# Kernel tuning notes

Hardware: AMD Instinct MI355X
Metric: run time of the kernel (lower is better)

## Reference

```python
import jax, jax.numpy as jnp
import numpy as np

EPS = 1e-7  # keras.backend.epsilon()


def setup_inputs() -> dict:
    key = jax.random.key(0)
    k1, k2 = jax.random.split(key)
    B, S, D = 8, 1024, 768
    # scale down: module exponentiates raw dot products with no max-subtraction
    input_a = jax.random.normal(k1, (B, S, D), dtype=jnp.float32) * 0.05
    input_mask = jax.random.randint(k2, (B, S), 0, 2, dtype=jnp.int32)
    return {"input_a": input_a, "input_mask": input_mask}


def reference(input_a, input_mask):
    # e = exp(Q K^T) with Q = K = input_a, attend_type='dot' (no scaling)
    e = jnp.exp(jnp.einsum('bsd,btd->bst', input_a, input_a))  # [B,S,S]
    m = input_mask.astype(input_a.dtype)
    e = e * m[:, :, None] * m[:, None, :]  # mask rows and cols
    e = e / (jnp.sum(e, axis=-1, keepdims=True) + EPS)  # renormalize
    attend = jnp.einsum('bst,btd->bsd', e, input_a)  # V = input_a
    return attend
```

## Files before the change

### kernel.cpp

```cpp
#include <hip/hip_runtime.h>
#include <cstdint>
#include <cstddef>

#define BATCH 8
#define SEQ 1024
#define DIM 768
#define EPS_K 1e-7f

typedef __bf16 bf16x8 __attribute__((ext_vector_type(8)));
typedef float f32x4 __attribute__((ext_vector_type(4)));

__device__ __forceinline__ uint16_t f2bf(float f) {
  union { float f; uint32_t u; } v; v.f = f;
  uint32_t u = v.u;
  u += 0x7FFFu + ((u >> 16) & 1u);
  return (uint16_t)(u >> 16);
}

__device__ __forceinline__ void gload16(const void* g, void* l) {
  __builtin_amdgcn_global_load_lds(
      (const __attribute__((address_space(1))) uint32_t*)g,
      (__attribute__((address_space(3))) uint32_t*)l, 16, 0, 0);
}

__global__ __launch_bounds__(256) void convert_kernel(const float* __restrict__ A,
                                                      uint16_t* __restrict__ ab,
                                                      uint16_t* __restrict__ at) {
  const int b  = blockIdx.z;
  const int s0 = blockIdx.y * 64;
  const int d0 = blockIdx.x * 64;
  __shared__ uint16_t tl[64][66];
  const int c  = threadIdx.x & 63;
  const int r0 = threadIdx.x >> 6;
  const float* Ab = A + (size_t)b * SEQ * DIM;
  uint16_t* abb = ab + (size_t)b * SEQ * DIM;
#pragma unroll
  for (int i = 0; i < 16; ++i) {
    int r = r0 + i * 4;
    uint16_t h = f2bf(Ab[(size_t)(s0 + r) * DIM + d0 + c]);
    abb[(size_t)(s0 + r) * DIM + d0 + c] = h;
    tl[r][c] = h;
  }
  __syncthreads();
  uint16_t* atb = at + (size_t)b * DIM * SEQ;
#pragma unroll
  for (int i = 0; i < 16; ++i) {
    int r = r0 + i * 4;
    atb[(size_t)(d0 + r) * SEQ + s0 + c] = tl[c][r];
  }
}

__global__ __launch_bounds__(256) void scores_kernel(const uint16_t* __restrict__ ab,
                                                     const int* __restrict__ mask,
                                                     uint16_t* __restrict__ P) {
  const int b    = blockIdx.x & 7;
  const int tile = blockIdx.x >> 3;
  const int s0   = (tile >> 3) * 128;
  const int t0   = (tile & 7) * 128;

  const int tid  = threadIdx.x;
  const int lane = tid & 63;
  const int wid  = tid >> 6;
  const int wr   = wid >> 1;
  const int wc   = wid & 1;

  __shared__ uint16_t ldsQ[2][128 * 32];
  __shared__ uint16_t ldsK[2][128 * 32];
  __shared__ float mrow[128];
  __shared__ float mcol[128];

  if (tid < 128)        mrow[tid]       = (float)mask[b * SEQ + s0 + tid];
  else                  mcol[tid - 128] = (float)mask[b * SEQ + t0 + (tid - 128)];

  const uint16_t* aQ = ab + (size_t)b * SEQ * DIM + (size_t)s0 * DIM;
  const uint16_t* aK = ab + (size_t)b * SEQ * DIM + (size_t)t0 * DIM;

  const int sr = (tid * 8) >> 5;
  const int sc = (tid * 8) & 31;
#define STAGE(buf, k0)                                                         \
  do {                                                                         \
    int _i0 = tid * 8, _i1 = (256 + tid) * 8;                                  \
    gload16(aQ + (size_t)sr * DIM + (k0) + sc,        &ldsQ[buf][_i0]);        \
    gload16(aQ + (size_t)(sr + 64) * DIM + (k0) + sc, &ldsQ[buf][_i1]);        \
    gload16(aK + (size_t)sr * DIM + (k0) + sc,        &ldsK[buf][_i0]);        \
    gload16(aK + (size_t)(sr + 64) * DIM + (k0) + sc, &ldsK[buf][_i1]);        \
  } while (0)

  f32x4 acc[4][4];
#pragma unroll
  for (int m = 0; m < 4; ++m)
#pragma unroll
    for (int n = 0; n < 4; ++n) acc[m][n] = f32x4{0.f, 0.f, 0.f, 0.f};

  STAGE(0, 0);
  __syncthreads();

  const int rowQ = wr * 64 + (lane & 15);
  const int rowK = wc * 64 + (lane & 15);
  const int kch  = (lane >> 4) * 8;

  int cur = 0;
  for (int k0 = 0; k0 < DIM; k0 += 32) {
    if (k0 + 32 < DIM) STAGE(cur ^ 1, k0 + 32);

    bf16x8 qf[4], kf[4];
#pragma unroll
    for (int m = 0; m < 4; ++m) qf[m] = *(const bf16x8*)&ldsQ[cur][(rowQ + m * 16) * 32 + kch];
#pragma unroll
    for (int n = 0; n < 4; ++n) kf[n] = *(const bf16x8*)&ldsK[cur][(rowK + n * 16) * 32 + kch];
#pragma unroll
    for (int m = 0; m < 4; ++m)
#pragma unroll
      for (int n = 0; n < 4; ++n)
        acc[m][n] = __builtin_amdgcn_mfma_f32_16x16x32_bf16(qf[m], kf[n], acc[m][n], 0, 0, 0);

    __syncthreads();
    cur ^= 1;
  }
#undef STAGE

  uint16_t* Pb = P + (size_t)b * SEQ * SEQ;
#pragma unroll
  for (int m = 0; m < 4; ++m) {
    const int qb = wr * 64 + m * 16 + (lane >> 4) * 4;
#pragma unroll
    for (int n = 0; n < 4; ++n) {
      const int tloc = wc * 64 + n * 16 + (lane & 15);
      const float mc = mcol[tloc];
#pragma unroll
      for (int j = 0; j < 4; ++j) {
        float e = __expf(acc[m][n][j]) * mrow[qb + j] * mc;
        Pb[(size_t)(s0 + qb + j) * SEQ + t0 + tloc] = f2bf(e);
      }
    }
  }
}

__global__ __launch_bounds__(256) void out_kernel(const uint16_t* __restrict__ P,
                                                  const uint16_t* __restrict__ at,
                                                  float* __restrict__ out) {
  const int b    = blockIdx.x & 7;
  const int tile = blockIdx.x >> 3;
  const int q0   = (tile / 6) * 128;
  const int d0   = (tile % 6) * 128;

  const int tid  = threadIdx.x;
  const int lane = tid & 63;
  const int wid  = tid >> 6;
  const int wr   = wid >> 1;
  const int wc   = wid & 1;

  __shared__ uint16_t ldsP[2][128 * 32];
  __shared__ uint16_t ldsA[2][128 * 32];

  const uint16_t* Pb = P  + (size_t)b * SEQ * SEQ + (size_t)q0 * SEQ;
  const uint16_t* Ab = at + (size_t)b * DIM * SEQ + (size_t)d0 * SEQ;

  const int sr = (tid * 8) >> 5;
  const int sc = (tid * 8) & 31;
#define STAGE(buf, k0)                                                         \
  do {                                                                         \
    int _i0 = tid * 8, _i1 = (256 + tid) * 8;                                  \
    gload16(Pb + (size_t)sr * SEQ + (k0) + sc,        &ldsP[buf][_i0]);        \
    gload16(Pb + (size_t)(sr + 64) * SEQ + (k0) + sc, &ldsP[buf][_i1]);        \
    gload16(Ab + (size_t)sr * SEQ + (k0) + sc,        &ldsA[buf][_i0]);        \
    gload16(Ab + (size_t)(sr + 64) * SEQ + (k0) + sc, &ldsA[buf][_i1]);        \
  } while (0)

  f32x4 acc[4][4];
  f32x4 accd[4];
#pragma unroll
  for (int m = 0; m < 4; ++m) {
    accd[m] = f32x4{0.f, 0.f, 0.f, 0.f};
#pragma unroll
    for (int n = 0; n < 4; ++n) acc[m][n] = f32x4{0.f, 0.f, 0.f, 0.f};
  }

  bf16x8 onesf;
#pragma unroll
  for (int i = 0; i < 8; ++i) onesf[i] = (__bf16)1.0f;

  STAGE(0, 0);
  __syncthreads();

  const int rowP = wr * 64 + (lane & 15);
  const int rowA = wc * 64 + (lane & 15);
  const int kch  = (lane >> 4) * 8;

  int cur = 0;
  for (int k0 = 0; k0 < SEQ; k0 += 32) {
    if (k0 + 32 < SEQ) STAGE(cur ^ 1, k0 + 32);

    bf16x8 pf[4], af[4];
#pragma unroll
    for (int m = 0; m < 4; ++m) pf[m] = *(const bf16x8*)&ldsP[cur][(rowP + m * 16) * 32 + kch];
#pragma unroll
    for (int n = 0; n < 4; ++n) af[n] = *(const bf16x8*)&ldsA[cur][(rowA + n * 16) * 32 + kch];
#pragma unroll
    for (int m = 0; m < 4; ++m) {
#pragma unroll
      for (int n = 0; n < 4; ++n)
        acc[m][n] = __builtin_amdgcn_mfma_f32_16x16x32_bf16(pf[m], af[n], acc[m][n], 0, 0, 0);
      accd[m] = __builtin_amdgcn_mfma_f32_16x16x32_bf16(pf[m], onesf, accd[m], 0, 0, 0);
    }

    __syncthreads();
    cur ^= 1;
  }
#undef STAGE

  float* ob = out + (size_t)b * SEQ * DIM;
#pragma unroll
  for (int m = 0; m < 4; ++m) {
#pragma unroll
    for (int j = 0; j < 4; ++j) {
      const int ql = wr * 64 + m * 16 + (lane >> 4) * 4 + j;
      const float sc2 = 1.0f / (accd[m][j] + EPS_K);
#pragma unroll
      for (int n = 0; n < 4; ++n) {
        const int dl = d0 + wc * 64 + n * 16 + (lane & 15);
        ob[(size_t)(q0 + ql) * DIM + dl] = acc[m][n][j] * sc2;
      }
    }
  }
}

extern "C" void kernel_launch(void* const* d_in, const int* in_sizes, int n_in,
                              void* d_out, int out_size, void* d_ws, size_t ws_size,
                              hipStream_t stream) {
  (void)in_sizes; (void)n_in; (void)out_size; (void)ws_size;
  const float* A    = (const float*)d_in[0];
  const int*   mask = (const int*)d_in[1];
  float*       out  = (float*)d_out;

  char* ws = (char*)d_ws;
  const size_t NB_AB = (size_t)BATCH * SEQ * DIM * 2;
  const size_t NB_AT = NB_AB;
  uint16_t* ab = (uint16_t*)(ws);
  uint16_t* at = (uint16_t*)(ws + NB_AB);
  uint16_t* P  = (uint16_t*)(ws + NB_AB + NB_AT);

  dim3 blk(256);
  convert_kernel<<<dim3(DIM / 64, SEQ / 64, BATCH), blk, 0, stream>>>(A, ab, at);
  scores_kernel<<<dim3(64 * BATCH), blk, 0, stream>>>(ab, mask, P);
  out_kernel<<<dim3(48 * BATCH), blk, 0, stream>>>(P, at, out);
}
```

Baseline: 118.6 us.

## Enlarge GEMM tiles, swizzle LDS, deepen K step, vectorize conversion

Both GEMM kernels move to 512-thread blocks with 256x128 output tiles and a 64-wide K step. LDS columns are XOR-swizzled to avoid bank conflicts, and explicit vmcnt waits, raw barriers and setprio are meant to overlap the prefetch with MFMA work. The convert kernel now uses vectorized float4 loads and 16-byte bf16 stores for both the copy and the transpose. The grid shrinks to 256 and 192 blocks, which may underfill the 256 CUs, and the larger tiles raise register and LDS pressure.

```diff
diff --git a/kernel.cpp b/kernel.cpp
--- a/kernel.cpp
+++ b/kernel.cpp
@@ -9,6 +9,7 @@
 
 typedef __bf16 bf16x8 __attribute__((ext_vector_type(8)));
 typedef float f32x4 __attribute__((ext_vector_type(4)));
+typedef uint16_t u16x8 __attribute__((ext_vector_type(8)));
 
 __device__ __forceinline__ uint16_t f2bf(float f) {
   union { float f; uint32_t u; } v; v.f = f;
@@ -29,33 +30,41 @@
   const int b  = blockIdx.z;
   const int s0 = blockIdx.y * 64;
   const int d0 = blockIdx.x * 64;
-  __shared__ uint16_t tl[64][66];
-  const int c  = threadIdx.x & 63;
-  const int r0 = threadIdx.x >> 6;
-  const float* Ab = A + (size_t)b * SEQ * DIM;
-  uint16_t* abb = ab + (size_t)b * SEQ * DIM;
-#pragma unroll
-  for (int i = 0; i < 16; ++i) {
-    int r = r0 + i * 4;
-    uint16_t h = f2bf(Ab[(size_t)(s0 + r) * DIM + d0 + c]);
-    abb[(size_t)(s0 + r) * DIM + d0 + c] = h;
-    tl[r][c] = h;
+  __shared__ uint16_t tl[64][80];
+  const int tid = threadIdx.x;
+
+#pragma unroll
+  for (int i = 0; i < 2; ++i) {
+    const int sl = (tid >> 3) + i * 32;
+    const int ch = tid & 7;
+    const float* src = A + ((size_t)b * SEQ + s0 + sl) * DIM + d0 + ch * 8;
+    float4 f0 = *(const float4*)src;
+    float4 f1 = *(const float4*)(src + 4);
+    u16x8 h;
+    h[0] = f2bf(f0.x); h[1] = f2bf(f0.y); h[2] = f2bf(f0.z); h[3] = f2bf(f0.w);
+    h[4] = f2bf(f1.x); h[5] = f2bf(f1.y); h[6] = f2bf(f1.z); h[7] = f2bf(f1.w);
+    *(u16x8*)&ab[((size_t)b * SEQ + s0 + sl) * DIM + d0 + ch * 8] = h;
+    *(u16x8*)&tl[sl][ch * 8] = h;
   }
   __syncthreads();
-  uint16_t* atb = at + (size_t)b * DIM * SEQ;
-#pragma unroll
-  for (int i = 0; i < 16; ++i) {
-    int r = r0 + i * 4;
-    atb[(size_t)(d0 + r) * SEQ + s0 + c] = tl[c][r];
-  }
-}
-
-__global__ __launch_bounds__(256) void scores_kernel(const uint16_t* __restrict__ ab,
-                                                     const int* __restrict__ mask,
-                                                     uint16_t* __restrict__ P) {
+  const int dl = tid >> 2;
+#pragma unroll
+  for (int i = 0; i < 2; ++i) {
+    const int sc = (tid & 3) + i * 4;
+    u16x8 h;
+#pragma unroll
+    for (int e = 0; e < 8; ++e) h[e] = tl[sc * 8 + e][dl];
+    *(u16x8*)&at[((size_t)b * DIM + d0 + dl) * SEQ + s0 + sc * 8] = h;
+  }
+}
+
+
+__global__ __launch_bounds__(512, 2) void scores_kernel(const uint16_t* __restrict__ ab,
+                                                        const int* __restrict__ mask,
+                                                        uint16_t* __restrict__ P) {
   const int b    = blockIdx.x & 7;
   const int tile = blockIdx.x >> 3;
-  const int s0   = (tile >> 3) * 128;
+  const int s0   = (tile >> 3) * 256;
   const int t0   = (tile & 7) * 128;
 
   const int tid  = threadIdx.x;
@@ -64,26 +73,26 @@
   const int wr   = wid >> 1;
   const int wc   = wid & 1;
 
-  __shared__ uint16_t ldsQ[2][128 * 32];
-  __shared__ uint16_t ldsK[2][128 * 32];
-  __shared__ float mrow[128];
-  __shared__ float mcol[128];
-
-  if (tid < 128)        mrow[tid]       = (float)mask[b * SEQ + s0 + tid];
-  else                  mcol[tid - 128] = (float)mask[b * SEQ + t0 + (tid - 128)];
-
-  const uint16_t* aQ = ab + (size_t)b * SEQ * DIM + (size_t)s0 * DIM;
-  const uint16_t* aK = ab + (size_t)b * SEQ * DIM + (size_t)t0 * DIM;
-
-  const int sr = (tid * 8) >> 5;
-  const int sc = (tid * 8) & 31;
+  __shared__ __align__(16) uint16_t lA[2][256 * 64];
+  __shared__ __align__(16) uint16_t lB[2][128 * 64];
+
+  const uint16_t* gA = ab + ((size_t)b * SEQ + s0) * DIM;
+  const uint16_t* gB = ab + ((size_t)b * SEQ + t0) * DIM;
+
+  const int srl  = tid >> 3;
+  const int schx = ((tid & 7) ^ (srl & 7)) << 3;
+  const int sdst = srl * 64 + (tid & 7) * 8;
+
 #define STAGE(buf, k0)                                                         \
   do {                                                                         \
-    int _i0 = tid * 8, _i1 = (256 + tid) * 8;                                  \
-    gload16(aQ + (size_t)sr * DIM + (k0) + sc,        &ldsQ[buf][_i0]);        \
-    gload16(aQ + (size_t)(sr + 64) * DIM + (k0) + sc, &ldsQ[buf][_i1]);        \
-    gload16(aK + (size_t)sr * DIM + (k0) + sc,        &ldsK[buf][_i0]);        \
-    gload16(aK + (size_t)(sr + 64) * DIM + (k0) + sc, &ldsK[buf][_i1]);        \
+    _Pragma("unroll")                                                          \
+    for (int _i = 0; _i < 4; ++_i)                                             \
+      gload16(gA + (size_t)(srl + _i * 64) * DIM + (k0) + schx,                \
+              &lA[buf][sdst + _i * 64 * 64]);                                  \
+    _Pragma("unroll")                                                          \
+    for (int _i = 0; _i < 2; ++_i)                                             \
+      gload16(gB + (size_t)(srl + _i * 64) * DIM + (k0) + schx,                \
+              &lB[buf][sdst + _i * 64 * 64]);                                  \
   } while (0)
 
   f32x4 acc[4][4];
@@ -92,56 +101,72 @@
 #pragma unroll
     for (int n = 0; n < 4; ++n) acc[m][n] = f32x4{0.f, 0.f, 0.f, 0.f};
 
+  const int rA  = wr * 64 + (lane & 15);
+  const int rB  = wc * 64 + (lane & 15);
+  const int cx0 = (((lane >> 4) + 0) ^ (lane & 7)) << 3;
+  const int cx1 = (((lane >> 4) + 4) ^ (lane & 7)) << 3;
+
   STAGE(0, 0);
-  __syncthreads();
-
-  const int rowQ = wr * 64 + (lane & 15);
-  const int rowK = wc * 64 + (lane & 15);
-  const int kch  = (lane >> 4) * 8;
-
   int cur = 0;
-  for (int k0 = 0; k0 < DIM; k0 += 32) {
-    if (k0 + 32 < DIM) STAGE(cur ^ 1, k0 + 32);
-
-    bf16x8 qf[4], kf[4];
-#pragma unroll
-    for (int m = 0; m < 4; ++m) qf[m] = *(const bf16x8*)&ldsQ[cur][(rowQ + m * 16) * 32 + kch];
-#pragma unroll
-    for (int n = 0; n < 4; ++n) kf[n] = *(const bf16x8*)&ldsK[cur][(rowK + n * 16) * 32 + kch];
-#pragma unroll
-    for (int m = 0; m < 4; ++m)
-#pragma unroll
-      for (int n = 0; n < 4; ++n)
-        acc[m][n] = __builtin_amdgcn_mfma_f32_16x16x32_bf16(qf[m], kf[n], acc[m][n], 0, 0, 0);
-
-    __syncthreads();
+  for (int t = 0; t < DIM / 64; ++t) {
+    if (t + 1 < DIM / 64) {
+      STAGE(cur ^ 1, (t + 1) * 64);
+      asm volatile("s_waitcnt vmcnt(6)" ::: "memory");
+    } else {
+      asm volatile("s_waitcnt vmcnt(0)" ::: "memory");
+    }
+    __builtin_amdgcn_s_barrier();
+
+    bf16x8 bfr[2][4];
+#pragma unroll
+    for (int n = 0; n < 4; ++n) {
+      bfr[0][n] = *(const bf16x8*)&lB[cur][(rB + n * 16) * 64 + cx0];
+      bfr[1][n] = *(const bf16x8*)&lB[cur][(rB + n * 16) * 64 + cx1];
+    }
+    __builtin_amdgcn_s_setprio(1);
+#pragma unroll
+    for (int m = 0; m < 4; ++m) {
+      bf16x8 a0 = *(const bf16x8*)&lA[cur][(rA + m * 16) * 64 + cx0];
+      bf16x8 a1 = *(const bf16x8*)&lA[cur][(rA + m * 16) * 64 + cx1];
+#pragma unroll
+      for (int n = 0; n < 4; ++n) {
+        acc[m][n] = __builtin_amdgcn_mfma_f32_16x16x32_bf16(a0, bfr[0][n], acc[m][n], 0, 0, 0);
+        acc[m][n] = __builtin_amdgcn_mfma_f32_16x16x32_bf16(a1, bfr[1][n], acc[m][n], 0, 0, 0);
+      }
+    }
+    __builtin_amdgcn_s_setprio(0);
+    __builtin_amdgcn_s_barrier();
     cur ^= 1;
   }
 #undef STAGE
 
+  const int* mk = mask + b * SEQ;
   uint16_t* Pb = P + (size_t)b * SEQ * SEQ;
+  float mc[4];
+#pragma unroll
+  for (int n = 0; n < 4; ++n) mc[n] = (float)mk[t0 + wc * 64 + n * 16 + (lane & 15)];
 #pragma unroll
   for (int m = 0; m < 4; ++m) {
-    const int qb = wr * 64 + m * 16 + (lane >> 4) * 4;
-#pragma unroll
-    for (int n = 0; n < 4; ++n) {
-      const int tloc = wc * 64 + n * 16 + (lane & 15);
-      const float mc = mcol[tloc];
-#pragma unroll
-      for (int j = 0; j < 4; ++j) {
-        float e = __expf(acc[m][n][j]) * mrow[qb + j] * mc;
-        Pb[(size_t)(s0 + qb + j) * SEQ + t0 + tloc] = f2bf(e);
-      }
-    }
-  }
-}
-
-__global__ __launch_bounds__(256) void out_kernel(const uint16_t* __restrict__ P,
-                                                  const uint16_t* __restrict__ at,
-                                                  float* __restrict__ out) {
+#pragma unroll
+    for (int j = 0; j < 4; ++j) {
+      const int rs = s0 + wr * 64 + m * 16 + (lane >> 4) * 4 + j;
+      const float mr = (float)mk[rs];
+#pragma unroll
+      for (int n = 0; n < 4; ++n) {
+        const int ct = t0 + wc * 64 + n * 16 + (lane & 15);
+        float e = __expf(acc[m][n][j]) * mr * mc[n];
+        Pb[(size_t)rs * SEQ + ct] = f2bf(e);
+      }
+    }
+  }
+}
+
+__global__ __launch_bounds__(512, 2) void out_kernel(const uint16_t* __restrict__ P,
+                                                     const uint16_t* __restrict__ at,
+                                                     float* __restrict__ out) {
   const int b    = blockIdx.x & 7;
   const int tile = blockIdx.x >> 3;
-  const int q0   = (tile / 6) * 128;
+  const int q0   = (tile / 6) * 256;
   const int d0   = (tile % 6) * 128;
 
   const int tid  = threadIdx.x;
@@ -150,21 +175,26 @@
   const int wr   = wid >> 1;
   const int wc   = wid & 1;
 
-  __shared__ uint16_t ldsP[2][128 * 32];
-  __shared__ uint16_t ldsA[2][128 * 32];
-
-  const uint16_t* Pb = P  + (size_t)b * SEQ * SEQ + (size_t)q0 * SEQ;
-  const uint16_t* Ab = at + (size_t)b * DIM * SEQ + (size_t)d0 * SEQ;
-
-  const int sr = (tid * 8) >> 5;
-  const int sc = (tid * 8) & 31;
+  __shared__ __align__(16) uint16_t lA[2][256 * 64];
+  __shared__ __align__(16) uint16_t lB[2][128 * 64];
+
+  const uint16_t* gA = P  + ((size_t)b * SEQ + q0) * SEQ;
+  const uint16_t* gB = at + ((size_t)b * DIM + d0) * SEQ;
+
+  const int srl  = tid >> 3;
+  const int schx = ((tid & 7) ^ (srl & 7)) << 3;
+  const int sdst = srl * 64 + (tid & 7) * 8;
+
 #define STAGE(buf, k0)                                                         \
   do {                                                                         \
-    int _i0 = tid * 8, _i1 = (256 + tid) * 8;                                  \
-    gload16(Pb + (size_t)sr * SEQ + (k0) + sc,        &ldsP[buf][_i0]);        \
-    gload16(Pb + (size_t)(sr + 64) * SEQ + (k0) + sc, &ldsP[buf][_i1]);        \
-    gload16(Ab + (size_t)sr * SEQ + (k0) + sc,        &ldsA[buf][_i0]);        \
-    gload16(Ab + (size_t)(sr + 64) * SEQ + (k0) + sc, &ldsA[buf][_i1]);        \
+    _Pragma("unroll")                                                          \
+    for (int _i = 0; _i < 4; ++_i)                                             \
+      gload16(gA + (size_t)(srl + _i * 64) * SEQ + (k0) + schx,                \
+              &lA[buf][sdst + _i * 64 * 64]);                                  \
+    _Pragma("unroll")                                                          \
+    for (int _i = 0; _i < 2; ++_i)                                             \
+      gload16(gB + (size_t)(srl + _i * 64) * SEQ + (k0) + schx,                \
+              &lB[buf][sdst + _i * 64 * 64]);                                  \
   } while (0)
 
   f32x4 acc[4][4];
@@ -175,36 +205,47 @@
 #pragma unroll
     for (int n = 0; n < 4; ++n) acc[m][n] = f32x4{0.f, 0.f, 0.f, 0.f};
   }
-
-  bf16x8 onesf;
-#pragma unroll
-  for (int i = 0; i < 8; ++i) onesf[i] = (__bf16)1.0f;
+  bf16x8 ones;
+#pragma unroll
+  for (int i = 0; i < 8; ++i) ones[i] = (__bf16)1.0f;
+
+  const int rA  = wr * 64 + (lane & 15);
+  const int rB  = wc * 64 + (lane & 15);
+  const int cx0 = (((lane >> 4) + 0) ^ (lane & 7)) << 3;
+  const int cx1 = (((lane >> 4) + 4) ^ (lane & 7)) << 3;
 
   STAGE(0, 0);
-  __syncthreads();
-
-  const int rowP = wr * 64 + (lane & 15);
-  const int rowA = wc * 64 + (lane & 15);
-  const int kch  = (lane >> 4) * 8;
-
   int cur = 0;
-  for (int k0 = 0; k0 < SEQ; k0 += 32) {
-    if (k0 + 32 < SEQ) STAGE(cur ^ 1, k0 + 32);
-
-    bf16x8 pf[4], af[4];
-#pragma unroll
-    for (int m = 0; m < 4; ++m) pf[m] = *(const bf16x8*)&ldsP[cur][(rowP + m * 16) * 32 + kch];
-#pragma unroll
-    for (int n = 0; n < 4; ++n) af[n] = *(const bf16x8*)&ldsA[cur][(rowA + n * 16) * 32 + kch];
+  for (int t = 0; t < SEQ / 64; ++t) {
+    if (t + 1 < SEQ / 64) {
+      STAGE(cur ^ 1, (t + 1) * 64);
+      asm volatile("s_waitcnt vmcnt(6)" ::: "memory");
+    } else {
+      asm volatile("s_waitcnt vmcnt(0)" ::: "memory");
+    }
+    __builtin_amdgcn_s_barrier();
+
+    bf16x8 bfr[2][4];
+#pragma unroll
+    for (int n = 0; n < 4; ++n) {
+      bfr[0][n] = *(const bf16x8*)&lB[cur][(rB + n * 16) * 64 + cx0];
+      bfr[1][n] = *(const bf16x8*)&lB[cur][(rB + n * 16) * 64 + cx1];
+    }
+    __builtin_amdgcn_s_setprio(1);
 #pragma unroll
     for (int m = 0; m < 4; ++m) {
-#pragma unroll
-      for (int n = 0; n < 4; ++n)
-        acc[m][n] = __builtin_amdgcn_mfma_f32_16x16x32_bf16(pf[m], af[n], acc[m][n], 0, 0, 0);
-      accd[m] = __builtin_amdgcn_mfma_f32_16x16x32_bf16(pf[m], onesf, accd[m], 0, 0, 0);
-    }
-
-    __syncthreads();
+      bf16x8 a0 = *(const bf16x8*)&lA[cur][(rA + m * 16) * 64 + cx0];
+      bf16x8 a1 = *(const bf16x8*)&lA[cur][(rA + m * 16) * 64 + cx1];
+#pragma unroll
+      for (int n = 0; n < 4; ++n) {
+        acc[m][n] = __builtin_amdgcn_mfma_f32_16x16x32_bf16(a0, bfr[0][n], acc[m][n], 0, 0, 0);
+        acc[m][n] = __builtin_amdgcn_mfma_f32_16x16x32_bf16(a1, bfr[1][n], acc[m][n], 0, 0, 0);
+      }
+      accd[m] = __builtin_amdgcn_mfma_f32_16x16x32_bf16(a0, ones, accd[m], 0, 0, 0);
+      accd[m] = __builtin_amdgcn_mfma_f32_16x16x32_bf16(a1, ones, accd[m], 0, 0, 0);
+    }
+    __builtin_amdgcn_s_setprio(0);
+    __builtin_amdgcn_s_barrier();
     cur ^= 1;
   }
 #undef STAGE
@@ -214,12 +255,12 @@
   for (int m = 0; m < 4; ++m) {
 #pragma unroll
     for (int j = 0; j < 4; ++j) {
-      const int ql = wr * 64 + m * 16 + (lane >> 4) * 4 + j;
-      const float sc2 = 1.0f / (accd[m][j] + EPS_K);
-#pragma unroll
-      for (int n = 0; n < 4; ++n) {
-        const int dl = d0 + wc * 64 + n * 16 + (lane & 15);
-        ob[(size_t)(q0 + ql) * DIM + dl] = acc[m][n][j] * sc2;
+      const int q  = q0 + wr * 64 + m * 16 + (lane >> 4) * 4 + j;
+      const float sc = 1.0f / (accd[m][j] + EPS_K);
+#pragma unroll
+      for (int n = 0; n < 4; ++n) {
+        const int d = d0 + wc * 64 + n * 16 + (lane & 15);
+        ob[(size_t)q * DIM + d] = acc[m][n][j] * sc;
       }
     }
   }
@@ -240,8 +281,7 @@
   uint16_t* at = (uint16_t*)(ws + NB_AB);
   uint16_t* P  = (uint16_t*)(ws + NB_AB + NB_AT);
 
-  dim3 blk(256);
-  convert_kernel<<<dim3(DIM / 64, SEQ / 64, BATCH), blk, 0, stream>>>(A, ab, at);
-  scores_kernel<<<dim3(64 * BATCH), blk, 0, stream>>>(ab, mask, P);
-  out_kernel<<<dim3(48 * BATCH), blk, 0, stream>>>(P, at, out);
-}
+  convert_kernel<<<dim3(DIM / 64, SEQ / 64, BATCH), dim3(256), 0, stream>>>(A, ab, at);
+  scores_kernel<<<dim3(32 * BATCH), dim3(512), 0, stream>>>(ab, mask, P);
+  out_kernel<<<dim3(24 * BATCH), dim3(512), 0, stream>>>(P, at, out);
+}
```

Result: slower. 124.5 us (+5.0%).
